# Kernel optimization log

Hardware: AMD Instinct MI355X
Metric: run time of the kernel (lower is better)

## Reference

```python
import jax, jax.numpy as jnp
import numpy as np

N_NODES = 100000
IN_DIM = 64
HIDDEN = 128
N_EDGES = 1600000


def sage_conv(x, src, dst, W_l, W_r, b):
    # PyG SAGEConv (mean aggr): out = lin_l(mean_{j in N(i)} x_j) + lin_r(x_i) + bias
    agg = jax.ops.segment_sum(x[src], dst, num_segments=N_NODES)  # [N, d]
    cnt = jax.ops.segment_sum(jnp.ones((src.shape[0],), x.dtype), dst,
                              num_segments=N_NODES)  # [N]
    mean = agg / jnp.maximum(cnt, 1.0)[:, None]
    return mean @ W_l + x @ W_r + b


def setup_inputs() -> dict:
    key = jax.random.key(0)
    ks = jax.random.split(key, 10)
    x = jax.random.normal(ks[0], (N_NODES, IN_DIM), dtype=jnp.float32)
    edge_index = jax.random.randint(ks[1], (2, N_EDGES), 0, N_NODES, dtype=jnp.int64)
    s = 1.0 / np.sqrt(IN_DIM)
    W_l1 = jax.random.uniform(ks[2], (IN_DIM, HIDDEN), jnp.float32, -s, s)
    W_r1 = jax.random.uniform(ks[3], (IN_DIM, HIDDEN), jnp.float32, -s, s)
    b1 = jnp.zeros((HIDDEN,), jnp.float32)
    s2 = 1.0 / np.sqrt(HIDDEN)
    W_l2 = jax.random.uniform(ks[4], (HIDDEN, HIDDEN), jnp.float32, -s2, s2)
    W_r2 = jax.random.uniform(ks[5], (HIDDEN, HIDDEN), jnp.float32, -s2, s2)
    b2 = jnp.zeros((HIDDEN,), jnp.float32)
    W_out = jax.random.uniform(ks[6], (HIDDEN, 1), jnp.float32, -s2, s2)
    b_out = jnp.zeros((1,), jnp.float32)
    return {"x": x, "edge_index": edge_index,
            "W_l1": W_l1, "W_r1": W_r1, "b1": b1,
            "W_l2": W_l2, "W_r2": W_r2, "b2": b2,
            "W_out": W_out, "b_out": b_out}


def reference(x, edge_index, W_l1, W_r1, b1, W_l2, W_r2, b2, W_out, b_out):
    src, dst = edge_index[0], edge_index[1]
    h1 = jax.nn.relu(sage_conv(x, src, dst, W_l1, W_r1, b1))   # [N, H]
    h2 = sage_conv(h1, src, dst, W_l2, W_r2, b2)               # [N, H]
    out = (h2 @ W_out + b_out).squeeze(-1)                     # [N]
    return out, h1, h2
```

## Files before the change

kernel.cpp:

```cpp
#include <hip/hip_runtime.h>

#define NN 100000
#define IND 64
#define HID 128
#define NE 1600000

#define BKT2 256
#define NBKT2 ((NN + BKT2 - 1) / BKT2)
#define CAP 4992
#define EPB 4096
#define NBLK_E ((NE + EPB - 1) / EPB)

#define SCAN_CHUNK 1024
#define NSB ((NN + SCAN_CHUNK - 1) / SCAN_CHUNK)

typedef __attribute__((ext_vector_type(8))) short bf16x8;
typedef __attribute__((ext_vector_type(4))) float f32x4;
typedef __attribute__((ext_vector_type(2))) float f32x2;

static __device__ __forceinline__ unsigned short f2bf(float f) {
    unsigned u = __float_as_uint(f);
    u = (u + 0x7FFFu + ((u >> 16) & 1u)) >> 16;
    return (unsigned short)u;
}
static __device__ __forceinline__ unsigned pack2(float a, float b) {
    return (unsigned)f2bf(a) | ((unsigned)f2bf(b) << 16);
}


__global__ __launch_bounds__(512) void zero_small_kernel(int* __restrict__ p, int n) {
    int i = threadIdx.x;
    if (i < n) p[i] = 0;
}

__global__ __launch_bounds__(512) void binA_kernel(const int* __restrict__ src,
                                                   const int* __restrict__ dst,
                                                   int* __restrict__ bktcur,
                                                   unsigned* __restrict__ bins) {
    __shared__ int hcnt[NBKT2];
    __shared__ int rbase[NBKT2];
    int t = threadIdx.x;
    int e0 = blockIdx.x * EPB;
    int ce = min(EPB, NE - e0);
    for (int i = t; i < NBKT2; i += 512) hcnt[i] = 0;
    __syncthreads();
    for (int i = t; i < ce; i += 512)
        atomicAdd(&hcnt[dst[e0 + i] >> 8], 1);
    __syncthreads();
    for (int i = t; i < NBKT2; i += 512) {
        int c = hcnt[i];
        rbase[i] = c ? atomicAdd(&bktcur[i], c) : 0;
        hcnt[i] = 0;
    }
    __syncthreads();
    for (int i = t; i < ce; i += 512) {
        int d = dst[e0 + i];
        int b = d >> 8;
        int r = atomicAdd(&hcnt[b], 1);
        bins[(size_t)b * CAP + rbase[b] + r] =
            (unsigned)src[e0 + i] | ((unsigned)(d & 255) << 17);
    }
}

__global__ __launch_bounds__(256) void binB_kernel(const int* __restrict__ bktcur,
                                                   unsigned* __restrict__ bins,
                                                   int* __restrict__ cnt,
                                                   int* __restrict__ off) {
    __shared__ unsigned ebuf[CAP];
    __shared__ int ncnt[BKT2];
    __shared__ int nofs[BKT2];
    __shared__ int wtot[4];
    int t = threadIdx.x, lane = t & 63, w = t >> 6;
    int b = blockIdx.x;
    int m = bktcur[b];
    size_t base = (size_t)b * CAP;
    for (int i = t; i < m; i += 256) ebuf[i] = bins[base + i];
    ncnt[t] = 0;
    __syncthreads();
    for (int i = t; i < m; i += 256)
        atomicAdd(&ncnt[ebuf[i] >> 17], 1);
    __syncthreads();
    int v = ncnt[t];
    int incl = v;
    #pragma unroll
    for (int o = 1; o < 64; o <<= 1) {
        int u = __shfl_up(incl, o);
        if (lane >= o) incl += u;
    }
    if (lane == 63) wtot[w] = incl;
    __syncthreads();
    int wbase = 0;
    #pragma unroll
    for (int i = 0; i < 4; ++i) if (i < w) wbase += wtot[i];
    int ex = wbase + incl - v;
    nofs[t] = ex;
    int node = b * BKT2 + t;
    if (node < NN) { cnt[node] = v; off[node] = (int)base + ex; }
    __syncthreads();
    for (int i = t; i < m; i += 256) {
        unsigned val = ebuf[i];
        int r = atomicAdd(&nofs[val >> 17], 1);
        bins[base + r] = val & 0x1FFFFu;
    }
}


__global__ __launch_bounds__(256) void cvt_xq_kernel(const float4* __restrict__ x,
                                                     unsigned* __restrict__ xq) {
    int i = blockIdx.x * 256 + threadIdx.x;
    float4 v = x[i];
    int u = __builtin_amdgcn_cvt_pk_fp8_f32(v.x, v.y, 0, false);
    u = __builtin_amdgcn_cvt_pk_fp8_f32(v.z, v.w, u, true);
    xq[i] = (unsigned)u;
}

__global__ __launch_bounds__(256) void packW_kernel(const float* __restrict__ Wr,
                                                    const float* __restrict__ Wl,
                                                    int Khalf, int KS,
                                                    unsigned short* __restrict__ Wp) {
    int t = blockIdx.x * 256 + threadIdx.x;
    if (t >= 8 * KS * 64) return;
    int l  = t & 63;
    int ks = (t >> 6) % KS;
    int jt = t / (64 * KS);
    int j  = jt * 16 + (l & 15);
    int kb = ks * 32 + (l >> 4) * 8;
    unsigned short v[8];
    #pragma unroll
    for (int i = 0; i < 8; ++i) {
        int k = kb + i;
        float w = (k < Khalf) ? Wr[k * HID + j] : Wl[(k - Khalf) * HID + j];
        v[i] = f2bf(w);
    }
    ushort4 lo, hi;
    lo.x = v[0]; lo.y = v[1]; lo.z = v[2]; lo.w = v[3];
    hi.x = v[4]; hi.y = v[5]; hi.z = v[6]; hi.w = v[7];
    ushort4* d = reinterpret_cast<ushort4*>(Wp + (size_t)t * 8);
    d[0] = lo; d[1] = hi;
}


__global__ __launch_bounds__(256) void agg1_kernel(const unsigned char* __restrict__ xq,
                                                   const int* __restrict__ srcs,
                                                   const int* __restrict__ off,
                                                   const int* __restrict__ cnt,
                                                   unsigned short* __restrict__ m1b) {
    int t = threadIdx.x;
    int n = blockIdx.x * 4 + (t >> 6);
    int l = t & 63, ep = l >> 4, d4 = (l & 15) * 4;
    int s0 = off[n], deg = cnt[n];
    float a0 = 0.f, a1 = 0.f, a2 = 0.f, a3 = 0.f;
    int e = ep;
    for (; e + 4 < deg; e += 8) {
        int sA = srcs[s0 + e], sB = srcs[s0 + e + 4];
        unsigned uA = *reinterpret_cast<const unsigned*>(xq + (size_t)sA * IND + d4);
        unsigned uB = *reinterpret_cast<const unsigned*>(xq + (size_t)sB * IND + d4);
        f32x2 lA = __builtin_amdgcn_cvt_pk_f32_fp8((int)uA, false);
        f32x2 hA = __builtin_amdgcn_cvt_pk_f32_fp8((int)uA, true);
        f32x2 lB = __builtin_amdgcn_cvt_pk_f32_fp8((int)uB, false);
        f32x2 hB = __builtin_amdgcn_cvt_pk_f32_fp8((int)uB, true);
        a0 += lA.x + lB.x; a1 += lA.y + lB.y;
        a2 += hA.x + hB.x; a3 += hA.y + hB.y;
    }
    for (; e < deg; e += 4) {
        int s = srcs[s0 + e];
        unsigned u = *reinterpret_cast<const unsigned*>(xq + (size_t)s * IND + d4);
        f32x2 lo = __builtin_amdgcn_cvt_pk_f32_fp8((int)u, false);
        f32x2 hi = __builtin_amdgcn_cvt_pk_f32_fp8((int)u, true);
        a0 += lo.x; a1 += lo.y; a2 += hi.x; a3 += hi.y;
    }
    a0 += __shfl_down(a0, 32); a1 += __shfl_down(a1, 32);
    a2 += __shfl_down(a2, 32); a3 += __shfl_down(a3, 32);
    a0 += __shfl_down(a0, 16); a1 += __shfl_down(a1, 16);
    a2 += __shfl_down(a2, 16); a3 += __shfl_down(a3, 16);
    if (l < 16) {
        float inv = 1.f / fmaxf((float)deg, 1.f);
        uint2 o;
        o.x = pack2(a0 * inv, a1 * inv);
        o.y = pack2(a2 * inv, a3 * inv);
        *reinterpret_cast<uint2*>(m1b + (size_t)n * IND + d4) = o;
    }
}

__global__ __launch_bounds__(256) void agg2_kernel(const unsigned char* __restrict__ h1q,
                                                   const int* __restrict__ srcs,
                                                   const int* __restrict__ off,
                                                   const int* __restrict__ cnt,
                                                   unsigned short* __restrict__ m2b) {
    int t = threadIdx.x;
    int n = blockIdx.x * 4 + (t >> 6);
    int l = t & 63, ep = l >> 5, d4 = (l & 31) * 4;
    int s0 = off[n], deg = cnt[n];
    float a0 = 0.f, a1 = 0.f, a2 = 0.f, a3 = 0.f;
    int e = ep;
    for (; e + 6 < deg; e += 8) {
        int sA = srcs[s0 + e],     sB = srcs[s0 + e + 2];
        int sC = srcs[s0 + e + 4], sD = srcs[s0 + e + 6];
        unsigned uA = *reinterpret_cast<const unsigned*>(h1q + (size_t)sA * HID + d4);
        unsigned uB = *reinterpret_cast<const unsigned*>(h1q + (size_t)sB * HID + d4);
        unsigned uC = *reinterpret_cast<const unsigned*>(h1q + (size_t)sC * HID + d4);
        unsigned uD = *reinterpret_cast<const unsigned*>(h1q + (size_t)sD * HID + d4);
        f32x2 lA = __builtin_amdgcn_cvt_pk_f32_fp8((int)uA, false);
        f32x2 hA = __builtin_amdgcn_cvt_pk_f32_fp8((int)uA, true);
        f32x2 lB = __builtin_amdgcn_cvt_pk_f32_fp8((int)uB, false);
        f32x2 hB = __builtin_amdgcn_cvt_pk_f32_fp8((int)uB, true);
        f32x2 lC = __builtin_amdgcn_cvt_pk_f32_fp8((int)uC, false);
        f32x2 hC = __builtin_amdgcn_cvt_pk_f32_fp8((int)uC, true);
        f32x2 lD = __builtin_amdgcn_cvt_pk_f32_fp8((int)uD, false);
        f32x2 hD = __builtin_amdgcn_cvt_pk_f32_fp8((int)uD, true);
        a0 += (lA.x + lB.x) + (lC.x + lD.x);
        a1 += (lA.y + lB.y) + (lC.y + lD.y);
        a2 += (hA.x + hB.x) + (hC.x + hD.x);
        a3 += (hA.y + hB.y) + (hC.y + hD.y);
    }
    for (; e < deg; e += 2) {
        int s = srcs[s0 + e];
        unsigned u = *reinterpret_cast<const unsigned*>(h1q + (size_t)s * HID + d4);
        f32x2 lo = __builtin_amdgcn_cvt_pk_f32_fp8((int)u, false);
        f32x2 hi = __builtin_amdgcn_cvt_pk_f32_fp8((int)u, true);
        a0 += lo.x; a1 += lo.y; a2 += hi.x; a3 += hi.y;
    }
    a0 += __shfl_down(a0, 32); a1 += __shfl_down(a1, 32);
    a2 += __shfl_down(a2, 32); a3 += __shfl_down(a3, 32);
    if (l < 32) {
        float inv = 1.f / fmaxf((float)deg, 1.f);
        uint2 o;
        o.x = pack2(a0 * inv, a1 * inv);
        o.y = pack2(a2 * inv, a3 * inv);
        *reinterpret_cast<uint2*>(m2b + (size_t)n * HID + d4) = o;
    }
}


__global__ __launch_bounds__(256) void mfma1_kernel(const float* __restrict__ x,
                                                    const unsigned short* __restrict__ m1b,
                                                    const unsigned short* __restrict__ Wp,
                                                    const float* __restrict__ b,
                                                    float* __restrict__ h1f,
                                                    unsigned short* __restrict__ h1b,
                                                    unsigned char* __restrict__ h1q) {
    int t = threadIdx.x, w = t >> 6, l = t & 63;
    int row0 = blockIdx.x * 64 + w * 16;
    int arow = row0 + (l & 15); if (arow > NN - 1) arow = NN - 1;
    int kcol = (l >> 4) * 8;
    f32x4 acc[8];
    #pragma unroll
    for (int jt = 0; jt < 8; ++jt) { acc[jt][0] = 0.f; acc[jt][1] = 0.f; acc[jt][2] = 0.f; acc[jt][3] = 0.f; }
    #pragma unroll
    for (int ks = 0; ks < 4; ++ks) {
        bf16x8 a;
        int c = (ks & 1) * 32 + kcol;
        if (ks < 2) {
            const float* xr = x + (size_t)arow * IND + c;
            float4 f0 = *reinterpret_cast<const float4*>(xr);
            float4 f1 = *reinterpret_cast<const float4*>(xr + 4);
            a[0] = (short)f2bf(f0.x); a[1] = (short)f2bf(f0.y);
            a[2] = (short)f2bf(f0.z); a[3] = (short)f2bf(f0.w);
            a[4] = (short)f2bf(f1.x); a[5] = (short)f2bf(f1.y);
            a[6] = (short)f2bf(f1.z); a[7] = (short)f2bf(f1.w);
        } else {
            a = *reinterpret_cast<const bf16x8*>(m1b + (size_t)arow * IND + c);
        }
        #pragma unroll
        for (int jt = 0; jt < 8; ++jt) {
            bf16x8 bb = *reinterpret_cast<const bf16x8*>(Wp + ((size_t)(jt * 4 + ks) * 64 + l) * 8);
            acc[jt] = __builtin_amdgcn_mfma_f32_16x16x32_bf16(a, bb, acc[jt], 0, 0, 0);
        }
    }
    int rbase = row0 + (l >> 4) * 4;
    #pragma unroll
    for (int jt = 0; jt < 8; ++jt) {
        int col = jt * 16 + (l & 15);
        float bias = b[col];
        #pragma unroll
        for (int r = 0; r < 4; ++r) {
            int row = rbase + r;
            if (row < NN) {
                float v = fmaxf(acc[jt][r] + bias, 0.f);
                h1f[(size_t)row * HID + col] = v;
                h1b[(size_t)row * HID + col] = f2bf(v);
                unsigned q8 = (unsigned)__builtin_amdgcn_cvt_pk_fp8_f32(v, 0.f, 0, false) & 0xFFu;
                h1q[(size_t)row * HID + col] = (unsigned char)q8;
            }
        }
    }
}

__global__ __launch_bounds__(256) void mfma2_kernel(const unsigned short* __restrict__ h1b,
                                                    const unsigned short* __restrict__ m2b,
                                                    const unsigned short* __restrict__ Wp,
                                                    const float* __restrict__ b,
                                                    const float* __restrict__ Wout,
                                                    const float* __restrict__ bout,
                                                    float* __restrict__ h2f,
                                                    float* __restrict__ out) {
    int t = threadIdx.x, w = t >> 6, l = t & 63;
    int row0 = blockIdx.x * 64 + w * 16;
    int arow = row0 + (l & 15); if (arow > NN - 1) arow = NN - 1;
    int kcol = (l >> 4) * 8;
    f32x4 acc[8];
    #pragma unroll
    for (int jt = 0; jt < 8; ++jt) { acc[jt][0] = 0.f; acc[jt][1] = 0.f; acc[jt][2] = 0.f; acc[jt][3] = 0.f; }
    #pragma unroll
    for (int ks = 0; ks < 8; ++ks) {
        const unsigned short* A = (ks < 4) ? h1b : m2b;
        int c = (ks & 3) * 32 + kcol;
        bf16x8 a = *reinterpret_cast<const bf16x8*>(A + (size_t)arow * HID + c);
        #pragma unroll
        for (int jt = 0; jt < 8; ++jt) {
            bf16x8 bb = *reinterpret_cast<const bf16x8*>(Wp + ((size_t)(jt * 8 + ks) * 64 + l) * 8);
            acc[jt] = __builtin_amdgcn_mfma_f32_16x16x32_bf16(a, bb, acc[jt], 0, 0, 0);
        }
    }
    int rbase = row0 + (l >> 4) * 4;
    float hs0 = 0.f, hs1 = 0.f, hs2 = 0.f, hs3 = 0.f;
    #pragma unroll
    for (int jt = 0; jt < 8; ++jt) {
        int col = jt * 16 + (l & 15);
        float bias = b[col];
        float wo = Wout[col];
        #pragma unroll
        for (int r = 0; r < 4; ++r) {
            int row = rbase + r;
            float v = acc[jt][r] + bias;
            if (row < NN) h2f[(size_t)row * HID + col] = v;
            if (r == 0) hs0 += v * wo;
            else if (r == 1) hs1 += v * wo;
            else if (r == 2) hs2 += v * wo;
            else hs3 += v * wo;
        }
    }
    #pragma unroll
    for (int o = 1; o < 16; o <<= 1) {
        hs0 += __shfl_xor(hs0, o);
        hs1 += __shfl_xor(hs1, o);
        hs2 += __shfl_xor(hs2, o);
        hs3 += __shfl_xor(hs3, o);
    }
    if ((l & 15) == 0) {
        float bo = bout[0];
        if (rbase + 0 < NN) out[rbase + 0] = hs0 + bo;
        if (rbase + 1 < NN) out[rbase + 1] = hs1 + bo;
        if (rbase + 2 < NN) out[rbase + 2] = hs2 + bo;
        if (rbase + 3 < NN) out[rbase + 3] = hs3 + bo;
    }
}


__global__ __launch_bounds__(256) void zero_int_kernel(int4* __restrict__ p, int n4) {
    int i = blockIdx.x * 256 + threadIdx.x;
    if (i < n4) p[i] = make_int4(0, 0, 0, 0);
}

__global__ __launch_bounds__(256) void hist_kernel(const int* __restrict__ dst,
                                                   int* __restrict__ cnt) {
    int e = blockIdx.x * 256 + threadIdx.x;
    if (e < NE) atomicAdd(&cnt[dst[e]], 1);
}

__global__ __launch_bounds__(256) void scanA_kernel(const int* __restrict__ cnt,
                                                    int* __restrict__ bsums) {
    int b = blockIdx.x, t = threadIdx.x;
    int base = b * SCAN_CHUNK + t * 4;
    int s = 0;
    #pragma unroll
    for (int k = 0; k < 4; ++k) { int i = base + k; if (i < NN) s += cnt[i]; }
    #pragma unroll
    for (int o = 32; o > 0; o >>= 1) s += __shfl_down(s, o);
    __shared__ int wsum[4];
    if ((t & 63) == 0) wsum[t >> 6] = s;
    __syncthreads();
    if (t == 0) bsums[b] = wsum[0] + wsum[1] + wsum[2] + wsum[3];
}

__global__ void scanB_kernel(int* __restrict__ bsums) {
    int acc = 0;
    for (int i = 0; i < NSB; ++i) { int v = bsums[i]; bsums[i] = acc; acc += v; }
}

__global__ __launch_bounds__(256) void scanC_kernel(const int* __restrict__ cnt,
                                                    const int* __restrict__ bsums,
                                                    int* __restrict__ off,
                                                    int* __restrict__ cur) {
    int b = blockIdx.x, t = threadIdx.x;
    int lane = t & 63, w = t >> 6;
    int base = b * SCAN_CHUNK + t * 4;
    int v[4]; int s = 0;
    #pragma unroll
    for (int k = 0; k < 4; ++k) {
        int i = base + k;
        v[k] = (i < NN) ? cnt[i] : 0;
        s += v[k];
    }
    int inc = s;
    #pragma unroll
    for (int o = 1; o < 64; o <<= 1) {
        int xv = __shfl_up(inc, o);
        if (lane >= o) inc += xv;
    }
    __shared__ int wsum[4];
    if (lane == 63) wsum[w] = inc;
    __syncthreads();
    int wbase = 0;
    for (int i = 0; i < w; ++i) wbase += wsum[i];
    int ex = bsums[b] + wbase + (inc - s);
    #pragma unroll
    for (int k = 0; k < 4; ++k) {
        int i = base + k;
        if (i < NN) { off[i] = ex; cur[i] = ex; }
        ex += v[k];
    }
}

__global__ __launch_bounds__(256) void fill_kernel(const int* __restrict__ src,
                                                   const int* __restrict__ dst,
                                                   int* __restrict__ cur,
                                                   int* __restrict__ srcs) {
    int e = blockIdx.x * 256 + threadIdx.x;
    if (e < NE) {
        int p = atomicAdd(&cur[dst[e]], 1);
        srcs[p] = src[e];
    }
}

__global__ __launch_bounds__(256) void agg1f_kernel(const float* __restrict__ x,
                                                    const int* __restrict__ srcs,
                                                    const int* __restrict__ off,
                                                    const int* __restrict__ cnt,
                                                    float* __restrict__ mean1) {
    int t = threadIdx.x;
    int n = blockIdx.x * 4 + (t >> 6);
    int d = t & 63;
    int s0 = off[n], deg = cnt[n];
    float acc = 0.f;
    for (int e = 0; e < deg; ++e) acc += x[(size_t)srcs[s0 + e] * IND + d];
    mean1[(size_t)n * HID + d] = acc / fmaxf((float)deg, 1.f);
}

__global__ __launch_bounds__(256) void agg2f_kernel(const float* __restrict__ h1,
                                                    const int* __restrict__ srcs,
                                                    const int* __restrict__ off,
                                                    const int* __restrict__ cnt,
                                                    float* __restrict__ mean2) {
    int t = threadIdx.x;
    int n = blockIdx.x * 2 + (t >> 7);
    int d = t & 127;
    int s0 = off[n], deg = cnt[n];
    float acc = 0.f;
    for (int e = 0; e < deg; ++e) acc += h1[(size_t)srcs[s0 + e] * HID + d];
    mean2[(size_t)n * HID + d] = acc / fmaxf((float)deg, 1.f);
}

__global__ __launch_bounds__(256) void gemm1f_kernel(const float* __restrict__ x,
                                                     const float* __restrict__ Wl,
                                                     const float* __restrict__ Wr,
                                                     const float* __restrict__ b,
                                                     float* __restrict__ h1) {
    __shared__ float in[16][128];
    int t = threadIdx.x;
    int node0 = blockIdx.x * 16;
    for (int idx = t; idx < 16 * 128; idx += 256) {
        int r = idx >> 7, c = idx & 127;
        in[r][c] = (c < IND) ? x[(size_t)(node0 + r) * IND + c]
                             : h1[(size_t)(node0 + r) * HID + (c - IND)];
    }
    __syncthreads();
    int j = t & 127, g = t >> 7;
    float acc[8];
    float bj = b[j];
    #pragma unroll
    for (int q = 0; q < 8; ++q) acc[q] = bj;
    for (int k = 0; k < 128; ++k) {
        float wv = (k < IND) ? Wr[k * HID + j] : Wl[(k - IND) * HID + j];
        #pragma unroll
        for (int q = 0; q < 8; ++q) acc[q] += in[g * 8 + q][k] * wv;
    }
    #pragma unroll
    for (int q = 0; q < 8; ++q)
        h1[(size_t)(node0 + g * 8 + q) * HID + j] = fmaxf(acc[q], 0.f);
}

__global__ __launch_bounds__(256) void gemm2f_kernel(const float* __restrict__ h1,
                                                     const float* __restrict__ Wl,
                                                     const float* __restrict__ Wr,
                                                     const float* __restrict__ b,
                                                     const float* __restrict__ Wout,
                                                     const float* __restrict__ bout,
                                                     float* __restrict__ h2,
                                                     float* __restrict__ out) {
    __shared__ float in[16][256];
    __shared__ float part[4][8];
    int t = threadIdx.x;
    int node0 = blockIdx.x * 16;
    for (int idx = t; idx < 16 * 256; idx += 256) {
        int r = idx >> 8, c = idx & 255;
        in[r][c] = (c < HID) ? h1[(size_t)(node0 + r) * HID + c]
                             : h2[(size_t)(node0 + r) * HID + (c - HID)];
    }
    __syncthreads();
    int j = t & 127, g = t >> 7, lane = t & 63, w = t >> 6;
    float acc[8];
    float bj = b[j];
    #pragma unroll
    for (int q = 0; q < 8; ++q) acc[q] = bj;
    for (int k = 0; k < 256; ++k) {
        float wv = (k < HID) ? Wr[k * HID + j] : Wl[(k - HID) * HID + j];
        #pragma unroll
        for (int q = 0; q < 8; ++q) acc[q] += in[g * 8 + q][k] * wv;
    }
    float wo = Wout[j];
    #pragma unroll
    for (int q = 0; q < 8; ++q)
        h2[(size_t)(node0 + g * 8 + q) * HID + j] = acc[q];
    #pragma unroll
    for (int q = 0; q < 8; ++q) {
        float v = acc[q] * wo;
        #pragma unroll
        for (int o = 32; o > 0; o >>= 1) v += __shfl_down(v, o);
        if (lane == 0) part[w][q] = v;
    }
    __syncthreads();
    if (t < 16) {
        int gg = t >> 3, q = t & 7;
        out[node0 + t] = part[2 * gg][q] + part[2 * gg + 1][q] + bout[0];
    }
}


extern "C" void kernel_launch(void* const* d_in, const int* in_sizes, int n_in,
                              void* d_out, int out_size, void* d_ws, size_t ws_size,
                              hipStream_t stream) {
    const float* x    = (const float*)d_in[0];
    const int*   eidx = (const int*)d_in[1];
    const int*   src  = eidx;
    const int*   dst  = eidx + NE;
    const float* Wl1  = (const float*)d_in[2];
    const float* Wr1  = (const float*)d_in[3];
    const float* b1   = (const float*)d_in[4];
    const float* Wl2  = (const float*)d_in[5];
    const float* Wr2  = (const float*)d_in[6];
    const float* b2   = (const float*)d_in[7];
    const float* Wout = (const float*)d_in[8];
    const float* bout = (const float*)d_in[9];

    float* out = (float*)d_out;
    float* h1f = out + NN;
    float* h2f = h1f + (size_t)NN * HID;

    char* p = (char*)d_ws;
    int* cnt        = (int*)p;            p += (size_t)NN * 4;
    int* off        = (int*)p;            p += (size_t)NN * 4;
    int* bktcur     = (int*)p;            p += 512 * 4;
    unsigned* bins  = (unsigned*)p;       p += (size_t)NBKT2 * CAP * 4;
    unsigned char* xq  = (unsigned char*)p;  p += (size_t)NN * IND;
    unsigned short* m1b = (unsigned short*)p; p += (size_t)NN * IND * 2;
    unsigned short* h1b = (unsigned short*)p; p += (size_t)NN * HID * 2;
    unsigned char* h1q  = (unsigned char*)p;  p += (size_t)NN * HID;
    unsigned short* m2b = (unsigned short*)p; p += (size_t)NN * HID * 2;
    unsigned short* Wp1 = (unsigned short*)p; p += 8 * 4 * 64 * 8 * 2;
    unsigned short* Wp2 = (unsigned short*)p; p += 8 * 8 * 64 * 8 * 2;
    const size_t need_v3 = (size_t)(p - (char*)d_ws);
    const size_t need_csr = ((size_t)3 * NN + 128 + NE) * sizeof(int);

    if (ws_size >= need_v3) {
        zero_small_kernel<<<1, 512, 0, stream>>>(bktcur, NBKT2);
        binA_kernel<<<NBLK_E, 512, 0, stream>>>(src, dst, bktcur, bins);
        binB_kernel<<<NBKT2, 256, 0, stream>>>(bktcur, bins, cnt, off);
        cvt_xq_kernel<<<(NN * IND / 4) / 256, 256, 0, stream>>>((const float4*)x, (unsigned*)xq);
        packW_kernel<<<8, 256, 0, stream>>>(Wr1, Wl1, IND, 4, Wp1);
        packW_kernel<<<16, 256, 0, stream>>>(Wr2, Wl2, HID, 8, Wp2);
        agg1_kernel<<<NN / 4, 256, 0, stream>>>(xq, (const int*)bins, off, cnt, m1b);
        mfma1_kernel<<<(NN + 63) / 64, 256, 0, stream>>>(x, m1b, Wp1, b1, h1f, h1b, h1q);
        agg2_kernel<<<NN / 4, 256, 0, stream>>>(h1q, (const int*)bins, off, cnt, m2b);
        mfma2_kernel<<<(NN + 63) / 64, 256, 0, stream>>>(h1b, m2b, Wp2, b2, Wout, bout, h2f, out);
    } else if (ws_size >= need_csr) {
        int* cntF   = (int*)d_ws;
        int* offF   = cntF + NN;
        int* curF   = offF + NN;
        int* bsums  = curF + NN;
        int* srcsF  = bsums + 128;
        zero_int_kernel<<<(NN / 4 + 255) / 256, 256, 0, stream>>>((int4*)cntF, NN / 4);
        hist_kernel<<<(NE + 255) / 256, 256, 0, stream>>>(dst, cntF);
        scanA_kernel<<<NSB, 256, 0, stream>>>(cntF, bsums);
        scanB_kernel<<<1, 1, 0, stream>>>(bsums);
        scanC_kernel<<<NSB, 256, 0, stream>>>(cntF, bsums, offF, curF);
        fill_kernel<<<(NE + 255) / 256, 256, 0, stream>>>(src, dst, curF, srcsF);
        agg1f_kernel<<<NN / 4, 256, 0, stream>>>(x, srcsF, offF, cntF, h1f);
        gemm1f_kernel<<<NN / 16, 256, 0, stream>>>(x, Wl1, Wr1, b1, h1f);
        agg2f_kernel<<<NN / 2, 256, 0, stream>>>(h1f, srcsF, offF, cntF, h2f);
        gemm2f_kernel<<<NN / 16, 256, 0, stream>>>(h1f, Wl2, Wr2, b2, Wout, bout, h2f, out);
    }
}
```

Measured before the change: 225.4 us.

## Merge prep kernels into one launch, widen binB blocks, deepen aggregation unroll

Folds the bucket-counter zeroing, fp8 conversion of x, and both weight-packing launches into a single prep kernel, which cuts three kernel launches. binB now runs 512 threads per block, with only the first 256 threads doing the per-node scan. The gather loops in agg1 and agg2 are unrolled to 4 and 8 loads in flight, to hide memory latency on the random neighbor reads. The risk is higher register use in the aggregation kernels, and an extra barrier in binB.

```diff
diff --git a/kernel.cpp b/kernel.cpp
--- a/kernel.cpp
+++ b/kernel.cpp
@@ -11,6 +11,10 @@
 #define EPB 4096
 #define NBLK_E ((NE + EPB - 1) / EPB)
 
+#define CVT_BLKS (NN * IND / 4 / 256)
+#define PW1_BLKS 8
+#define PW2_BLKS 16
+
 #define SCAN_CHUNK 1024
 #define NSB ((NN + SCAN_CHUNK - 1) / SCAN_CHUNK)
 
@@ -28,10 +32,56 @@
 }
 
 
-__global__ __launch_bounds__(512) void zero_small_kernel(int* __restrict__ p, int n) {
-    int i = threadIdx.x;
-    if (i < n) p[i] = 0;
-}
+static __device__ __forceinline__ void packW_body(const float* __restrict__ Wr,
+                                                  const float* __restrict__ Wl,
+                                                  int Khalf, int KS, int t,
+                                                  unsigned short* __restrict__ Wp) {
+    if (t >= 8 * KS * 64) return;
+    int l  = t & 63;
+    int ks = (t >> 6) % KS;
+    int jt = t / (64 * KS);
+    int j  = jt * 16 + (l & 15);
+    int kb = ks * 32 + (l >> 4) * 8;
+    unsigned short v[8];
+    #pragma unroll
+    for (int i = 0; i < 8; ++i) {
+        int k = kb + i;
+        float w = (k < Khalf) ? Wr[k * HID + j] : Wl[(k - Khalf) * HID + j];
+        v[i] = f2bf(w);
+    }
+    ushort4 lo, hi;
+    lo.x = v[0]; lo.y = v[1]; lo.z = v[2]; lo.w = v[3];
+    hi.x = v[4]; hi.y = v[5]; hi.z = v[6]; hi.w = v[7];
+    ushort4* d = reinterpret_cast<ushort4*>(Wp + (size_t)t * 8);
+    d[0] = lo; d[1] = hi;
+}
+
+__global__ __launch_bounds__(256) void prep_kernel(const float4* __restrict__ x,
+                                                   unsigned* __restrict__ xq,
+                                                   const float* __restrict__ Wr1,
+                                                   const float* __restrict__ Wl1,
+                                                   unsigned short* __restrict__ Wp1,
+                                                   const float* __restrict__ Wr2,
+                                                   const float* __restrict__ Wl2,
+                                                   unsigned short* __restrict__ Wp2,
+                                                   int* __restrict__ bktcur) {
+    int blk = blockIdx.x, t = threadIdx.x;
+    if (blk < CVT_BLKS) {
+        int i = blk * 256 + t;
+        float4 v = x[i];
+        int u = __builtin_amdgcn_cvt_pk_fp8_f32(v.x, v.y, 0, false);
+        u = __builtin_amdgcn_cvt_pk_fp8_f32(v.z, v.w, u, true);
+        xq[i] = (unsigned)u;
+    } else if (blk < CVT_BLKS + PW1_BLKS) {
+        packW_body(Wr1, Wl1, IND, 4, (blk - CVT_BLKS) * 256 + t, Wp1);
+    } else if (blk < CVT_BLKS + PW1_BLKS + PW2_BLKS) {
+        packW_body(Wr2, Wl2, HID, 8, (blk - CVT_BLKS - PW1_BLKS) * 256 + t, Wp2);
+    } else {
+        bktcur[t] = 0;
+        bktcur[t + 256] = 0;
+    }
+}
+
 
 __global__ __launch_bounds__(512) void binA_kernel(const int* __restrict__ src,
                                                    const int* __restrict__ dst,
@@ -62,7 +112,7 @@
     }
 }
 
-__global__ __launch_bounds__(256) void binB_kernel(const int* __restrict__ bktcur,
+__global__ __launch_bounds__(512) void binB_kernel(const int* __restrict__ bktcur,
                                                    unsigned* __restrict__ bins,
                                                    int* __restrict__ cnt,
                                                    int* __restrict__ off) {
@@ -74,69 +124,39 @@
     int b = blockIdx.x;
     int m = bktcur[b];
     size_t base = (size_t)b * CAP;
-    for (int i = t; i < m; i += 256) ebuf[i] = bins[base + i];
-    ncnt[t] = 0;
-    __syncthreads();
-    for (int i = t; i < m; i += 256)
+    for (int i = t; i < m; i += 512) ebuf[i] = bins[base + i];
+    if (t < BKT2) ncnt[t] = 0;
+    __syncthreads();
+    for (int i = t; i < m; i += 512)
         atomicAdd(&ncnt[ebuf[i] >> 17], 1);
     __syncthreads();
-    int v = ncnt[t];
-    int incl = v;
-    #pragma unroll
-    for (int o = 1; o < 64; o <<= 1) {
-        int u = __shfl_up(incl, o);
-        if (lane >= o) incl += u;
-    }
-    if (lane == 63) wtot[w] = incl;
-    __syncthreads();
-    int wbase = 0;
-    #pragma unroll
-    for (int i = 0; i < 4; ++i) if (i < w) wbase += wtot[i];
-    int ex = wbase + incl - v;
-    nofs[t] = ex;
-    int node = b * BKT2 + t;
-    if (node < NN) { cnt[node] = v; off[node] = (int)base + ex; }
-    __syncthreads();
-    for (int i = t; i < m; i += 256) {
+    if (t < BKT2) {
+        int v = ncnt[t];
+        int incl = v;
+        #pragma unroll
+        for (int o = 1; o < 64; o <<= 1) {
+            int u = __shfl_up(incl, o);
+            if (lane >= o) incl += u;
+        }
+        if (lane == 63) wtot[w] = incl;
+        nofs[t] = incl - v;
+    }
+    __syncthreads();
+    if (t < BKT2) {
+        int wbase = 0;
+        #pragma unroll
+        for (int i = 0; i < 4; ++i) if (i < w) wbase += wtot[i];
+        int ex = nofs[t] + wbase;
+        nofs[t] = ex;
+        int node = b * BKT2 + t;
+        if (node < NN) { cnt[node] = ncnt[t]; off[node] = (int)base + ex; }
+    }
+    __syncthreads();
+    for (int i = t; i < m; i += 512) {
         unsigned val = ebuf[i];
         int r = atomicAdd(&nofs[val >> 17], 1);
         bins[base + r] = val & 0x1FFFFu;
     }
-}
-
-
-__global__ __launch_bounds__(256) void cvt_xq_kernel(const float4* __restrict__ x,
-                                                     unsigned* __restrict__ xq) {
-    int i = blockIdx.x * 256 + threadIdx.x;
-    float4 v = x[i];
-    int u = __builtin_amdgcn_cvt_pk_fp8_f32(v.x, v.y, 0, false);
-    u = __builtin_amdgcn_cvt_pk_fp8_f32(v.z, v.w, u, true);
-    xq[i] = (unsigned)u;
-}
-
-__global__ __launch_bounds__(256) void packW_kernel(const float* __restrict__ Wr,
-                                                    const float* __restrict__ Wl,
-                                                    int Khalf, int KS,
-                                                    unsigned short* __restrict__ Wp) {
-    int t = blockIdx.x * 256 + threadIdx.x;
-    if (t >= 8 * KS * 64) return;
-    int l  = t & 63;
-    int ks = (t >> 6) % KS;
-    int jt = t / (64 * KS);
-    int j  = jt * 16 + (l & 15);
-    int kb = ks * 32 + (l >> 4) * 8;
-    unsigned short v[8];
-    #pragma unroll
-    for (int i = 0; i < 8; ++i) {
-        int k = kb + i;
-        float w = (k < Khalf) ? Wr[k * HID + j] : Wl[(k - Khalf) * HID + j];
-        v[i] = f2bf(w);
-    }
-    ushort4 lo, hi;
-    lo.x = v[0]; lo.y = v[1]; lo.z = v[2]; lo.w = v[3];
-    hi.x = v[4]; hi.y = v[5]; hi.z = v[6]; hi.w = v[7];
-    ushort4* d = reinterpret_cast<ushort4*>(Wp + (size_t)t * 8);
-    d[0] = lo; d[1] = hi;
 }
 
 
@@ -151,55 +171,13 @@
     int s0 = off[n], deg = cnt[n];
     float a0 = 0.f, a1 = 0.f, a2 = 0.f, a3 = 0.f;
     int e = ep;
-    for (; e + 4 < deg; e += 8) {
-        int sA = srcs[s0 + e], sB = srcs[s0 + e + 4];
+    for (; e + 12 < deg; e += 16) {
+        int sA = srcs[s0 + e],     sB = srcs[s0 + e + 4];
+        int sC = srcs[s0 + e + 8], sD = srcs[s0 + e + 12];
         unsigned uA = *reinterpret_cast<const unsigned*>(xq + (size_t)sA * IND + d4);
         unsigned uB = *reinterpret_cast<const unsigned*>(xq + (size_t)sB * IND + d4);
-        f32x2 lA = __builtin_amdgcn_cvt_pk_f32_fp8((int)uA, false);
-        f32x2 hA = __builtin_amdgcn_cvt_pk_f32_fp8((int)uA, true);
-        f32x2 lB = __builtin_amdgcn_cvt_pk_f32_fp8((int)uB, false);
-        f32x2 hB = __builtin_amdgcn_cvt_pk_f32_fp8((int)uB, true);
-        a0 += lA.x + lB.x; a1 += lA.y + lB.y;
-        a2 += hA.x + hB.x; a3 += hA.y + hB.y;
-    }
-    for (; e < deg; e += 4) {
-        int s = srcs[s0 + e];
-        unsigned u = *reinterpret_cast<const unsigned*>(xq + (size_t)s * IND + d4);
-        f32x2 lo = __builtin_amdgcn_cvt_pk_f32_fp8((int)u, false);
-        f32x2 hi = __builtin_amdgcn_cvt_pk_f32_fp8((int)u, true);
-        a0 += lo.x; a1 += lo.y; a2 += hi.x; a3 += hi.y;
-    }
-    a0 += __shfl_down(a0, 32); a1 += __shfl_down(a1, 32);
-    a2 += __shfl_down(a2, 32); a3 += __shfl_down(a3, 32);
-    a0 += __shfl_down(a0, 16); a1 += __shfl_down(a1, 16);
-    a2 += __shfl_down(a2, 16); a3 += __shfl_down(a3, 16);
-    if (l < 16) {
-        float inv = 1.f / fmaxf((float)deg, 1.f);
-        uint2 o;
-        o.x = pack2(a0 * inv, a1 * inv);
-        o.y = pack2(a2 * inv, a3 * inv);
-        *reinterpret_cast<uint2*>(m1b + (size_t)n * IND + d4) = o;
-    }
-}
-
-__global__ __launch_bounds__(256) void agg2_kernel(const unsigned char* __restrict__ h1q,
-                                                   const int* __restrict__ srcs,
-                                                   const int* __restrict__ off,
-                                                   const int* __restrict__ cnt,
-                                                   unsigned short* __restrict__ m2b) {
-    int t = threadIdx.x;
-    int n = blockIdx.x * 4 + (t >> 6);
-    int l = t & 63, ep = l >> 5, d4 = (l & 31) * 4;
-    int s0 = off[n], deg = cnt[n];
-    float a0 = 0.f, a1 = 0.f, a2 = 0.f, a3 = 0.f;
-    int e = ep;
-    for (; e + 6 < deg; e += 8) {
-        int sA = srcs[s0 + e],     sB = srcs[s0 + e + 2];
-        int sC = srcs[s0 + e + 4], sD = srcs[s0 + e + 6];
-        unsigned uA = *reinterpret_cast<const unsigned*>(h1q + (size_t)sA * HID + d4);
-        unsigned uB = *reinterpret_cast<const unsigned*>(h1q + (size_t)sB * HID + d4);
-        unsigned uC = *reinterpret_cast<const unsigned*>(h1q + (size_t)sC * HID + d4);
-        unsigned uD = *reinterpret_cast<const unsigned*>(h1q + (size_t)sD * HID + d4);
+        unsigned uC = *reinterpret_cast<const unsigned*>(xq + (size_t)sC * IND + d4);
+        unsigned uD = *reinterpret_cast<const unsigned*>(xq + (size_t)sD * IND + d4);
         f32x2 lA = __builtin_amdgcn_cvt_pk_f32_fp8((int)uA, false);
         f32x2 hA = __builtin_amdgcn_cvt_pk_f32_fp8((int)uA, true);
         f32x2 lB = __builtin_amdgcn_cvt_pk_f32_fp8((int)uB, false);
@@ -212,6 +190,71 @@
         a1 += (lA.y + lB.y) + (lC.y + lD.y);
         a2 += (hA.x + hB.x) + (hC.x + hD.x);
         a3 += (hA.y + hB.y) + (hC.y + hD.y);
+    }
+    for (; e < deg; e += 4) {
+        int s = srcs[s0 + e];
+        unsigned u = *reinterpret_cast<const unsigned*>(xq + (size_t)s * IND + d4);
+        f32x2 lo = __builtin_amdgcn_cvt_pk_f32_fp8((int)u, false);
+        f32x2 hi = __builtin_amdgcn_cvt_pk_f32_fp8((int)u, true);
+        a0 += lo.x; a1 += lo.y; a2 += hi.x; a3 += hi.y;
+    }
+    a0 += __shfl_down(a0, 32); a1 += __shfl_down(a1, 32);
+    a2 += __shfl_down(a2, 32); a3 += __shfl_down(a3, 32);
+    a0 += __shfl_down(a0, 16); a1 += __shfl_down(a1, 16);
+    a2 += __shfl_down(a2, 16); a3 += __shfl_down(a3, 16);
+    if (l < 16) {
+        float inv = 1.f / fmaxf((float)deg, 1.f);
+        uint2 o;
+        o.x = pack2(a0 * inv, a1 * inv);
+        o.y = pack2(a2 * inv, a3 * inv);
+        *reinterpret_cast<uint2*>(m1b + (size_t)n * IND + d4) = o;
+    }
+}
+
+__global__ __launch_bounds__(256) void agg2_kernel(const unsigned char* __restrict__ h1q,
+                                                   const int* __restrict__ srcs,
+                                                   const int* __restrict__ off,
+                                                   const int* __restrict__ cnt,
+                                                   unsigned short* __restrict__ m2b) {
+    int t = threadIdx.x;
+    int n = blockIdx.x * 4 + (t >> 6);
+    int l = t & 63, ep = l >> 5, d4 = (l & 31) * 4;
+    int s0 = off[n], deg = cnt[n];
+    float a0 = 0.f, a1 = 0.f, a2 = 0.f, a3 = 0.f;
+    int e = ep;
+    for (; e + 14 < deg; e += 16) {
+        int sA = srcs[s0 + e],      sB = srcs[s0 + e + 2];
+        int sC = srcs[s0 + e + 4],  sD = srcs[s0 + e + 6];
+        int sE = srcs[s0 + e + 8],  sF = srcs[s0 + e + 10];
+        int sG = srcs[s0 + e + 12], sH = srcs[s0 + e + 14];
+        unsigned uA = *reinterpret_cast<const unsigned*>(h1q + (size_t)sA * HID + d4);
+        unsigned uB = *reinterpret_cast<const unsigned*>(h1q + (size_t)sB * HID + d4);
+        unsigned uC = *reinterpret_cast<const unsigned*>(h1q + (size_t)sC * HID + d4);
+        unsigned uD = *reinterpret_cast<const unsigned*>(h1q + (size_t)sD * HID + d4);
+        unsigned uE = *reinterpret_cast<const unsigned*>(h1q + (size_t)sE * HID + d4);
+        unsigned uF = *reinterpret_cast<const unsigned*>(h1q + (size_t)sF * HID + d4);
+        unsigned uG = *reinterpret_cast<const unsigned*>(h1q + (size_t)sG * HID + d4);
+        unsigned uH = *reinterpret_cast<const unsigned*>(h1q + (size_t)sH * HID + d4);
+        f32x2 lA = __builtin_amdgcn_cvt_pk_f32_fp8((int)uA, false);
+        f32x2 hA = __builtin_amdgcn_cvt_pk_f32_fp8((int)uA, true);
+        f32x2 lB = __builtin_amdgcn_cvt_pk_f32_fp8((int)uB, false);
+        f32x2 hB = __builtin_amdgcn_cvt_pk_f32_fp8((int)uB, true);
+        f32x2 lC = __builtin_amdgcn_cvt_pk_f32_fp8((int)uC, false);
+        f32x2 hC = __builtin_amdgcn_cvt_pk_f32_fp8((int)uC, true);
+        f32x2 lD = __builtin_amdgcn_cvt_pk_f32_fp8((int)uD, false);
+        f32x2 hD = __builtin_amdgcn_cvt_pk_f32_fp8((int)uD, true);
+        f32x2 lE = __builtin_amdgcn_cvt_pk_f32_fp8((int)uE, false);
+        f32x2 hE = __builtin_amdgcn_cvt_pk_f32_fp8((int)uE, true);
+        f32x2 lF = __builtin_amdgcn_cvt_pk_f32_fp8((int)uF, false);
+        f32x2 hF = __builtin_amdgcn_cvt_pk_f32_fp8((int)uF, true);
+        f32x2 lG = __builtin_amdgcn_cvt_pk_f32_fp8((int)uG, false);
+        f32x2 hG = __builtin_amdgcn_cvt_pk_f32_fp8((int)uG, true);
+        f32x2 lH = __builtin_amdgcn_cvt_pk_f32_fp8((int)uH, false);
+        f32x2 hH = __builtin_amdgcn_cvt_pk_f32_fp8((int)uH, true);
+        a0 += ((lA.x + lB.x) + (lC.x + lD.x)) + ((lE.x + lF.x) + (lG.x + lH.x));
+        a1 += ((lA.y + lB.y) + (lC.y + lD.y)) + ((lE.y + lF.y) + (lG.y + lH.y));
+        a2 += ((hA.x + hB.x) + (hC.x + hD.x)) + ((hE.x + hF.x) + (hG.x + hH.x));
+        a3 += ((hA.y + hB.y) + (hC.y + hD.y)) + ((hE.y + hF.y) + (hG.y + hH.y));
     }
     for (; e < deg; e += 2) {
         int s = srcs[s0 + e];
@@ -552,7 +595,7 @@
     int* off        = (int*)p;            p += (size_t)NN * 4;
     int* bktcur     = (int*)p;            p += 512 * 4;
     unsigned* bins  = (unsigned*)p;       p += (size_t)NBKT2 * CAP * 4;
-    unsigned char* xq  = (unsigned char*)p;  p += (size_t)NN * IND;
+    unsigned char* xq  = (unsigned char*)p;   p += (size_t)NN * IND;
     unsigned short* m1b = (unsigned short*)p; p += (size_t)NN * IND * 2;
     unsigned short* h1b = (unsigned short*)p; p += (size_t)NN * HID * 2;
     unsigned char* h1q  = (unsigned char*)p;  p += (size_t)NN * HID;
@@ -563,12 +606,10 @@
     const size_t need_csr = ((size_t)3 * NN + 128 + NE) * sizeof(int);
 
     if (ws_size >= need_v3) {
-        zero_small_kernel<<<1, 512, 0, stream>>>(bktcur, NBKT2);
+        prep_kernel<<<CVT_BLKS + PW1_BLKS + PW2_BLKS + 1, 256, 0, stream>>>(
+            (const float4*)x, (unsigned*)xq, Wr1, Wl1, Wp1, Wr2, Wl2, Wp2, bktcur);
         binA_kernel<<<NBLK_E, 512, 0, stream>>>(src, dst, bktcur, bins);
-        binB_kernel<<<NBKT2, 256, 0, stream>>>(bktcur, bins, cnt, off);
-        cvt_xq_kernel<<<(NN * IND / 4) / 256, 256, 0, stream>>>((const float4*)x, (unsigned*)xq);
-        packW_kernel<<<8, 256, 0, stream>>>(Wr1, Wl1, IND, 4, Wp1);
-        packW_kernel<<<16, 256, 0, stream>>>(Wr2, Wl2, HID, 8, Wp2);
+        binB_kernel<<<NBKT2, 512, 0, stream>>>(bktcur, bins, cnt, off);
         agg1_kernel<<<NN / 4, 256, 0, stream>>>(xq, (const int*)bins, off, cnt, m1b);
         mfma1_kernel<<<(NN + 63) / 64, 256, 0, stream>>>(x, m1b, Wp1, b1, h1f, h1b, h1q);
         agg2_kernel<<<NN / 4, 256, 0, stream>>>(h1q, (const int*)bins, off, cnt, m2b);
```

New measurement: 226.7 us. Within noise of the previous version (+0.6%).
